# Kernel optimization log

Measured on AMD Instinct MI355X. Metric: run time of the kernel, lower is better.

The kernel has to match this reference:

```python
import jax, jax.numpy as jnp
import numpy as np

B, S, IN, OUT = 4, 2048, 4096, 4096


def setup_inputs() -> dict:
    key = jax.random.key(0)
    kx, kw, kb = jax.random.split(key, 3)
    x = jax.random.randint(kx, (B, S, IN), -127, 128, dtype=jnp.int8)
    weight = jax.random.randint(kw, (OUT, IN), -127, 128, dtype=jnp.int8)
    # original module initializes bias to zeros(int32); use random int32 to exercise the add
    bias = jax.random.randint(kb, (1, OUT), -1000, 1000, dtype=jnp.int32)
    return {"x": x, "weight": weight, "bias": bias}


def reference(x, weight, bias):
    x_shape = x.shape
    x2 = x.reshape(-1, x_shape[-1])  # [tokens, IN], int8
    # dot_general with preferred_element_type=int32 -> int8 inputs, int32 accumulate
    y = jax.lax.dot_general(
        x2, weight,
        dimension_numbers=(((1,), (1,)), ((), ())),
        preferred_element_type=jnp.int32,
    )  # [tokens, OUT] int32
    y = y + bias  # broadcast [1, OUT] int32
    return y.reshape(*x_shape[:-1], -1)
```

## Files before the change

### kernel.cpp

```cpp
#include <hip/hip_runtime.h>
#include <stdint.h>

#define M_TOT 8192
#define N_TOT 4096
#define K_TOT 4096

typedef int v4i  __attribute__((ext_vector_type(4)));
typedef int v16i __attribute__((ext_vector_type(16)));

__device__ __forceinline__ void gload_lds16(const void* g, void* l) {
    __builtin_amdgcn_global_load_lds(
        (const __attribute__((address_space(1))) unsigned int*)g,
        (__attribute__((address_space(3))) unsigned int*)l,
        16, 0, 0);
}

#define WAIT_V8_L0() __builtin_amdgcn_s_waitcnt(0x0078)
#define WAIT_V0_L0() __builtin_amdgcn_s_waitcnt(0x0070)
#define WAIT_V8()    __builtin_amdgcn_s_waitcnt(0x0f78)
#define SBAR()       __builtin_amdgcn_s_barrier()
#define SFENCE()     __builtin_amdgcn_sched_barrier(0)

__global__ __launch_bounds__(256) void pack_i32_to_i8(
        const int4* __restrict__ src, int* __restrict__ dst, int n4) {
    int idx = blockIdx.x * 1024 + threadIdx.x;
#pragma unroll
    for (int u = 0; u < 4; ++u, idx += 256) {
        const int4 a = src[idx];
        dst[idx] = (a.x & 255) | ((a.y & 255) << 8) |
                   ((a.z & 255) << 16) | (a.w << 24);
    }
}

__global__ __launch_bounds__(256, 1) void i8gemm_bias(
        const signed char* __restrict__ x,
        const signed char* __restrict__ w,
        const int* __restrict__ bias,
        int* __restrict__ out) {
    __shared__ __align__(16) signed char la[3][256 * 64];
    __shared__ __align__(16) signed char lb[3][256 * 64];

    const int tid  = threadIdx.x;
    const int lane = tid & 63;
    const int wv   = tid >> 6;
    const int l31  = lane & 31;
    const int kh   = lane >> 5;
    const int wr   = wv >> 1;
    const int wc   = wv & 1;

    const int flat = blockIdx.y * gridDim.x + blockIdx.x;
    const int swz  = (flat & 7) * 64 + (flat >> 3);
    const int bn0  = (swz & 15) * 256;
    const int bm0  = (swz >> 4) * 256;

    int bv[4];
#pragma unroll
    for (int j = 0; j < 4; ++j) bv[j] = bias[bn0 + wc * 128 + j * 32 + l31];
    v16i acc[4][4];
#pragma unroll
    for (int i = 0; i < 4; ++i)
#pragma unroll
        for (int j = 0; j < 4; ++j)
#pragma unroll
            for (int r = 0; r < 16; ++r) acc[i][j][r] = bv[j];

    const int fc = (lane & 3) ^ ((lane >> 3) & 3);
    const signed char* pa = x + (long)(bm0 + wv * 64 + (lane >> 2)) * K_TOT + fc * 16;
    const signed char* pb = w + (long)(bn0 + wv * 64 + (lane >> 2)) * K_TOT + fc * 16;
    const int lbase = wv * 64 * 64;

    const int swr  = (l31 >> 1) & 3;
    const int aoff = (wr * 128 + l31) * 64;
    const int boff = (wc * 128 + l31) * 64;
    const int cs0  = ((kh    ) ^ swr) * 16;
    const int cs1  = ((2 + kh) ^ swr) * 16;

    signed char* A0 = &la[0][0]; signed char* A1 = &la[1][0]; signed char* A2 = &la[2][0];
    signed char* B0 = &lb[0][0]; signed char* B1 = &lb[1][0]; signed char* B2 = &lb[2][0];

#pragma unroll
    for (int i = 0; i < 4; ++i) {
        gload_lds16(pa + (long)i * 16 * K_TOT, A0 + lbase + i * 1024);
        gload_lds16(pb + (long)i * 16 * K_TOT, B0 + lbase + i * 1024);
    }
#pragma unroll
    for (int i = 0; i < 4; ++i) {
        gload_lds16(pa + 64 + (long)i * 16 * K_TOT, A1 + lbase + i * 1024);
        gload_lds16(pb + 64 + (long)i * 16 * K_TOT, B1 + lbase + i * 1024);
    }
    WAIT_V8();
    SBAR();
    SFENCE();

    v4i a0[4], b0[4], a1[4], b1[4];
#pragma unroll
    for (int i = 0; i < 4; ++i) {
        a0[i] = *(const v4i*)(A0 + aoff + i * 2048 + cs0);
        b0[i] = *(const v4i*)(B0 + boff + i * 2048 + cs0);
    }

    const int NT = K_TOT / 64;
    for (int kt = 0; kt < NT; ++kt) {
        SFENCE();
#pragma unroll
        for (int i = 0; i < 4; ++i) {
            a1[i] = *(const v4i*)(A0 + aoff + i * 2048 + cs1);
            b1[i] = *(const v4i*)(B0 + boff + i * 2048 + cs1);
        }
        SFENCE();
        if (kt + 2 < NT) {
            const long k0 = (long)(kt + 2) * 64;
#pragma unroll
            for (int i = 0; i < 4; ++i) {
                gload_lds16(pa + k0 + (long)i * 16 * K_TOT, A2 + lbase + i * 1024);
                gload_lds16(pb + k0 + (long)i * 16 * K_TOT, B2 + lbase + i * 1024);
            }
        }
        SFENCE();
#pragma unroll
        for (int i = 0; i < 4; ++i)
#pragma unroll
            for (int j = 0; j < 4; ++j)
                acc[i][j] = __builtin_amdgcn_mfma_i32_32x32x32_i8(
                    a0[i], b0[j], acc[i][j], 0, 0, 0);
        SFENCE();
        if (kt + 1 < NT) {
            if (kt + 2 < NT) { WAIT_V8_L0(); } else { WAIT_V0_L0(); }
            SFENCE();
            SBAR();
            SFENCE();
#pragma unroll
            for (int i = 0; i < 4; ++i) {
                a0[i] = *(const v4i*)(A1 + aoff + i * 2048 + cs0);
                b0[i] = *(const v4i*)(B1 + boff + i * 2048 + cs0);
            }
            SFENCE();
        }
#pragma unroll
        for (int i = 0; i < 4; ++i)
#pragma unroll
            for (int j = 0; j < 4; ++j)
                acc[i][j] = __builtin_amdgcn_mfma_i32_32x32x32_i8(
                    a1[i], b1[j], acc[i][j], 0, 0, 0);

        signed char* t;
        t = A0; A0 = A1; A1 = A2; A2 = t;
        t = B0; B0 = B1; B1 = B2; B2 = t;
    }

#pragma unroll
    for (int i = 0; i < 4; ++i) {
        const int mbase = bm0 + wr * 128 + i * 32 + 4 * kh;
#pragma unroll
        for (int j = 0; j < 4; ++j) {
            const int n = bn0 + wc * 128 + j * 32 + l31;
#pragma unroll
            for (int r = 0; r < 16; ++r) {
                const int m = mbase + (r & 3) + 8 * (r >> 2);
                out[(long)m * N_TOT + n] = acc[i][j][r];
            }
        }
    }
}

extern "C" void kernel_launch(void* const* d_in, const int* in_sizes, int n_in,
                              void* d_out, int out_size, void* d_ws, size_t ws_size,
                              hipStream_t stream) {
    const int* x32  = (const int*)d_in[0];
    const int* w32  = (const int*)d_in[1];
    const int* bias = (const int*)d_in[2];
    int*       out  = (int*)d_out;

    signed char* xp = (signed char*)d_ws;
    signed char* wp = (signed char*)d_ws + (size_t)M_TOT * K_TOT;

    const int n4x = (M_TOT * K_TOT) / 4;
    const int n4w = (N_TOT * K_TOT) / 4;
    pack_i32_to_i8<<<n4x / 1024, 256, 0, stream>>>((const int4*)x32, (int*)xp, n4x);
    pack_i32_to_i8<<<n4w / 1024, 256, 0, stream>>>((const int4*)w32, (int*)wp, n4w);

    dim3 grid(N_TOT / 256, M_TOT / 256);
    i8gemm_bias<<<grid, 256, 0, stream>>>(xp, wp, bias, out);
}
```

Measured before the change: 403.6 us.

## Use 8 waves per GEMM block, split loads around MFMAs, merge pack kernels

The GEMM block grows from 4 to 8 waves, arranged 2x4. Each wave now computes a 128x64 sub-tile, so per-thread accumulators and B fragments are halved, and the global-to-LDS copies are spread over more threads. The A and B prefetches are split and placed around the two MFMA halves, the barrier now runs every iteration, and s_setprio raises priority during the MFMA bursts. The two int32-to-int8 pack launches are merged into one kernel that writes 16-byte stores. The trade-off is more waves per CU and a different balance between LDS reads and MFMA work per wave, which could affect latency hiding.

```diff
diff --git a/kernel.cpp b/kernel.cpp
--- a/kernel.cpp
+++ b/kernel.cpp
@@ -15,24 +15,35 @@
         16, 0, 0);
 }
 
-#define WAIT_V8_L0() __builtin_amdgcn_s_waitcnt(0x0078)
+#define WAIT_V2_L0() __builtin_amdgcn_s_waitcnt(0x0072)
 #define WAIT_V0_L0() __builtin_amdgcn_s_waitcnt(0x0070)
-#define WAIT_V8()    __builtin_amdgcn_s_waitcnt(0x0f78)
+#define WAIT_V4()    __builtin_amdgcn_s_waitcnt(0x0f74)
 #define SBAR()       __builtin_amdgcn_s_barrier()
 #define SFENCE()     __builtin_amdgcn_sched_barrier(0)
 
-__global__ __launch_bounds__(256) void pack_i32_to_i8(
-        const int4* __restrict__ src, int* __restrict__ dst, int n4) {
-    int idx = blockIdx.x * 1024 + threadIdx.x;
+__global__ __launch_bounds__(256) void pack2(
+        const int4* __restrict__ xs, int4* __restrict__ xd,
+        const int4* __restrict__ ws, int4* __restrict__ wd) {
+    const int t = blockIdx.x * 256 + threadIdx.x;
 #pragma unroll
-    for (int u = 0; u < 4; ++u, idx += 256) {
-        const int4 a = src[idx];
-        dst[idx] = (a.x & 255) | ((a.y & 255) << 8) |
-                   ((a.z & 255) << 16) | (a.w << 24);
+    for (int it = 0; it < 6; ++it) {
+        const long g = (long)it * 524288 + t;
+        const int4* __restrict__ src = (it < 4) ? xs : ws;
+        int4* __restrict__ dst       = (it < 4) ? xd : wd;
+        const long o = (it < 4) ? g : g - 2097152;
+        int4 r;
+        int* rp = (int*)&r;
+#pragma unroll
+        for (int q = 0; q < 4; ++q) {
+            const int4 a = src[o * 4 + q];
+            rp[q] = (a.x & 255) | ((a.y & 255) << 8) |
+                    ((a.z & 255) << 16) | (a.w << 24);
+        }
+        dst[o] = r;
     }
 }
 
-__global__ __launch_bounds__(256, 1) void i8gemm_bias(
+__global__ __launch_bounds__(512, 2) void i8gemm_bias(
         const signed char* __restrict__ x,
         const signed char* __restrict__ w,
         const int* __restrict__ bias,
@@ -45,33 +56,33 @@
     const int wv   = tid >> 6;
     const int l31  = lane & 31;
     const int kh   = lane >> 5;
-    const int wr   = wv >> 1;
-    const int wc   = wv & 1;
+    const int wr   = wv >> 2;
+    const int wc   = wv & 3;
 
     const int flat = blockIdx.y * gridDim.x + blockIdx.x;
     const int swz  = (flat & 7) * 64 + (flat >> 3);
     const int bn0  = (swz & 15) * 256;
     const int bm0  = (swz >> 4) * 256;
 
-    int bv[4];
+    int bv[2];
 #pragma unroll
-    for (int j = 0; j < 4; ++j) bv[j] = bias[bn0 + wc * 128 + j * 32 + l31];
-    v16i acc[4][4];
+    for (int j = 0; j < 2; ++j) bv[j] = bias[bn0 + wc * 64 + j * 32 + l31];
+    v16i acc[4][2];
 #pragma unroll
     for (int i = 0; i < 4; ++i)
 #pragma unroll
-        for (int j = 0; j < 4; ++j)
+        for (int j = 0; j < 2; ++j)
 #pragma unroll
             for (int r = 0; r < 16; ++r) acc[i][j][r] = bv[j];
 
     const int fc = (lane & 3) ^ ((lane >> 3) & 3);
-    const signed char* pa = x + (long)(bm0 + wv * 64 + (lane >> 2)) * K_TOT + fc * 16;
-    const signed char* pb = w + (long)(bn0 + wv * 64 + (lane >> 2)) * K_TOT + fc * 16;
-    const int lbase = wv * 64 * 64;
+    const signed char* pa = x + (long)(bm0 + wv * 32 + (lane >> 2)) * K_TOT + fc * 16;
+    const signed char* pb = w + (long)(bn0 + wv * 32 + (lane >> 2)) * K_TOT + fc * 16;
+    const int lbase = wv * 32 * 64;
 
     const int swr  = (l31 >> 1) & 3;
     const int aoff = (wr * 128 + l31) * 64;
-    const int boff = (wc * 128 + l31) * 64;
+    const int boff = (wc * 64  + l31) * 64;
     const int cs0  = ((kh    ) ^ swr) * 16;
     const int cs1  = ((2 + kh) ^ swr) * 16;
 
@@ -79,67 +90,72 @@
     signed char* B0 = &lb[0][0]; signed char* B1 = &lb[1][0]; signed char* B2 = &lb[2][0];
 
 #pragma unroll
-    for (int i = 0; i < 4; ++i) {
+    for (int i = 0; i < 2; ++i) {
         gload_lds16(pa + (long)i * 16 * K_TOT, A0 + lbase + i * 1024);
         gload_lds16(pb + (long)i * 16 * K_TOT, B0 + lbase + i * 1024);
     }
 #pragma unroll
-    for (int i = 0; i < 4; ++i) {
+    for (int i = 0; i < 2; ++i) {
         gload_lds16(pa + 64 + (long)i * 16 * K_TOT, A1 + lbase + i * 1024);
         gload_lds16(pb + 64 + (long)i * 16 * K_TOT, B1 + lbase + i * 1024);
     }
-    WAIT_V8();
+    WAIT_V4();
     SBAR();
     SFENCE();
 
-    v4i a0[4], b0[4], a1[4], b1[4];
+    v4i a0[4], b0[2], a1[4], b1[2];
 #pragma unroll
-    for (int i = 0; i < 4; ++i) {
-        a0[i] = *(const v4i*)(A0 + aoff + i * 2048 + cs0);
-        b0[i] = *(const v4i*)(B0 + boff + i * 2048 + cs0);
-    }
+    for (int i = 0; i < 4; ++i) a0[i] = *(const v4i*)(A0 + aoff + i * 2048 + cs0);
+#pragma unroll
+    for (int j = 0; j < 2; ++j) b0[j] = *(const v4i*)(B0 + boff + j * 2048 + cs0);
 
     const int NT = K_TOT / 64;
     for (int kt = 0; kt < NT; ++kt) {
         SFENCE();
 #pragma unroll
-        for (int i = 0; i < 4; ++i) {
-            a1[i] = *(const v4i*)(A0 + aoff + i * 2048 + cs1);
-            b1[i] = *(const v4i*)(B0 + boff + i * 2048 + cs1);
+        for (int i = 0; i < 4; ++i) a1[i] = *(const v4i*)(A0 + aoff + i * 2048 + cs1);
+#pragma unroll
+        for (int j = 0; j < 2; ++j) b1[j] = *(const v4i*)(B0 + boff + j * 2048 + cs1);
+        SFENCE();
+        if (kt + 2 < NT) {
+            const long k0 = (long)(kt + 2) * 64;
+#pragma unroll
+            for (int i = 0; i < 2; ++i)
+                gload_lds16(pa + k0 + (long)i * 16 * K_TOT, A2 + lbase + i * 1024);
+        }
+        SFENCE();
+        __builtin_amdgcn_s_setprio(1);
+#pragma unroll
+        for (int i = 0; i < 4; ++i)
+#pragma unroll
+            for (int j = 0; j < 2; ++j)
+                acc[i][j] = __builtin_amdgcn_mfma_i32_32x32x32_i8(
+                    a0[i], b0[j], acc[i][j], 0, 0, 0);
+        __builtin_amdgcn_s_setprio(0);
+        SFENCE();
+        if (kt + 2 < NT) { WAIT_V2_L0(); } else { WAIT_V0_L0(); }
+        SFENCE();
+        SBAR();
+        SFENCE();
+        if (kt + 1 < NT) {
+#pragma unroll
+            for (int i = 0; i < 4; ++i) a0[i] = *(const v4i*)(A1 + aoff + i * 2048 + cs0);
+#pragma unroll
+            for (int j = 0; j < 2; ++j) b0[j] = *(const v4i*)(B1 + boff + j * 2048 + cs0);
         }
         SFENCE();
         if (kt + 2 < NT) {
             const long k0 = (long)(kt + 2) * 64;
 #pragma unroll
-            for (int i = 0; i < 4; ++i) {
-                gload_lds16(pa + k0 + (long)i * 16 * K_TOT, A2 + lbase + i * 1024);
+            for (int i = 0; i < 2; ++i)
                 gload_lds16(pb + k0 + (long)i * 16 * K_TOT, B2 + lbase + i * 1024);
-            }
         }
         SFENCE();
+        __builtin_amdgcn_s_setprio(1);
 #pragma unroll
         for (int i = 0; i < 4; ++i)
 #pragma unroll
-            for (int j = 0; j < 4; ++j)
-                acc[i][j] = __builtin_amdgcn_mfma_i32_32x32x32_i8(
-                    a0[i], b0[j], acc[i][j], 0, 0, 0);
-        SFENCE();
-        if (kt + 1 < NT) {
-            if (kt + 2 < NT) { WAIT_V8_L0(); } else { WAIT_V0_L0(); }
-            SFENCE();
-            SBAR();
-            SFENCE();
-#pragma unroll
-            for (int i = 0; i < 4; ++i) {
-                a0[i] = *(const v4i*)(A1 + aoff + i * 2048 + cs0);
-                b0[i] = *(const v4i*)(B1 + boff + i * 2048 + cs0);
-            }
-            SFENCE();
-        }
-#pragma unroll
-        for (int i = 0; i < 4; ++i)
-#pragma unroll
-            for (int j = 0; j < 4; ++j)
+            for (int j = 0; j < 2; ++j)
                 acc[i][j] = __builtin_amdgcn_mfma_i32_32x32x32_i8(
                     a1[i], b1[j], acc[i][j], 0, 0, 0);
 
@@ -152,8 +168,8 @@
     for (int i = 0; i < 4; ++i) {
         const int mbase = bm0 + wr * 128 + i * 32 + 4 * kh;
 #pragma unroll
-        for (int j = 0; j < 4; ++j) {
-            const int n = bn0 + wc * 128 + j * 32 + l31;
+        for (int j = 0; j < 2; ++j) {
+            const int n = bn0 + wc * 64 + j * 32 + l31;
 #pragma unroll
             for (int r = 0; r < 16; ++r) {
                 const int m = mbase + (r & 3) + 8 * (r >> 2);
@@ -174,11 +190,9 @@
     signed char* xp = (signed char*)d_ws;
     signed char* wp = (signed char*)d_ws + (size_t)M_TOT * K_TOT;
 
-    const int n4x = (M_TOT * K_TOT) / 4;
-    const int n4w = (N_TOT * K_TOT) / 4;
-    pack_i32_to_i8<<<n4x / 1024, 256, 0, stream>>>((const int4*)x32, (int*)xp, n4x);
-    pack_i32_to_i8<<<n4w / 1024, 256, 0, stream>>>((const int4*)w32, (int*)wp, n4w);
+    pack2<<<2048, 256, 0, stream>>>((const int4*)x32, (int4*)xp,
+                                    (const int4*)w32, (int4*)wp);
 
     dim3 grid(N_TOT / 256, M_TOT / 256);
-    i8gemm_bias<<<grid, 256, 0, stream>>>(xp, wp, bias, out);
+    i8gemm_bias<<<grid, 512, 0, stream>>>(xp, wp, bias, out);
 }
```

After: 395.7 us (median of 3 runs). No clear change (-2.0%).
